# Kernel tuning notes

Hardware: AMD Instinct MI355X
Metric: run time of the kernel (lower is better)

Reference implementation:

```python
import jax, jax.numpy as jnp
import numpy as np

DIM = 256
N_EMBED = 8192


def setup_inputs() -> dict:
    key = jax.random.key(0)
    k1, k2 = jax.random.split(key)
    inp = jax.random.normal(k1, (8, 4096, DIM), dtype=jnp.float32)
    embed = jax.random.normal(k2, (DIM, N_EMBED), dtype=jnp.float32)  # codebook [dim, n_embed]
    return {"input": inp, "embed": embed}


def reference(input, embed):
    # Flatten all leading dims into N code queries: [N, dim]
    flatten = input.reshape(-1, DIM)
    dist = (
        jnp.sum(flatten * flatten, axis=1, keepdims=True)
        - 2.0 * (flatten @ embed)
        + jnp.sum(embed * embed, axis=0, keepdims=True)
    )
    # (-dist).max(1) indices == argmin of dist
    embed_ind = jnp.argmin(dist, axis=1).reshape(input.shape[:-1])  # [B, T]
    # Embedding gather from codebook transpose: [B, T, dim]
    quantize = jnp.take(embed.T, embed_ind, axis=0)
    # Commitment loss (quantize detached)
    diff = jnp.mean(jnp.square(jax.lax.stop_gradient(quantize) - input))
    # Straight-through estimator
    quantize = input + jax.lax.stop_gradient(quantize - input)
    return quantize, diff, embed_ind
```

## Files before the change

### kernel.cpp

```cpp
#include <hip/hip_runtime.h>

#define DIM 256
#define NEMB 8192
#define NQ 32768
#define OUT_Q_ELEMS 8388608
#define NSEG 2
#define SEG_CODES 4096
#define CAP_H 32
#define MARGIN 1.0f

typedef __attribute__((ext_vector_type(8))) short short8;
typedef __attribute__((ext_vector_type(4))) float f32x4;
typedef unsigned int u32_as1 __attribute__((address_space(1)));
typedef unsigned int u32_as3 __attribute__((address_space(3)));

__device__ __forceinline__ unsigned short f2bf(float f) {
    unsigned u = __float_as_uint(f);
    u += 0x7FFFu + ((u >> 16) & 1u);
    return (unsigned short)(u >> 16);
}
__device__ __forceinline__ void gll16(const void* g, void* l) {
    __builtin_amdgcn_global_load_lds((const u32_as1*)g, (u32_as3*)l, 16, 0, 0);
}

__global__ void prep_kernel(const float* __restrict__ input,
                            const float* __restrict__ embed,
                            int* __restrict__ cnt2, double* __restrict__ ed,
                            float* __restrict__ ef, float* __restrict__ ebt,
                            unsigned short* __restrict__ Xc,
                            unsigned short* __restrict__ Ec,
                            double* __restrict__ pacc) {
    __shared__ float t[64][65];
    const int b = blockIdx.x;
    if (b < 512) {
        cnt2[b * 256 + threadIdx.x] = 0;
    } else if (b < 544) {
        if (b == 512 && threadIdx.x < 64) pacc[threadIdx.x] = 0.0;
        int j = (b - 512) * 256 + threadIdx.x;
        double s = 0.0;
        for (int d = 0; d < DIM; ++d) {
            double v = (double)embed[(size_t)d * NEMB + j];
            s += v * v;
        }
        ed[j] = s;
        ef[j] = (float)s;
    } else if (b < 1056) {
        const int bb = b - 544;
        const int bx = bb & 127, by = bb >> 7;
        const int tx = threadIdx.x & 63, ty = threadIdx.x >> 6;
#pragma unroll
        for (int i = 0; i < 16; ++i) {
            int d = by * 64 + ty * 16 + i;
            t[ty * 16 + i][tx] = embed[(size_t)d * NEMB + bx * 64 + tx];
        }
        __syncthreads();
#pragma unroll
        for (int i = 0; i < 16; ++i) {
            int c = bx * 64 + ty * 16 + i;
            ebt[(size_t)c * DIM + by * 64 + tx] = t[tx][ty * 16 + i];
        }
    } else if (b < 5152) {
        int tid = (b - 1056) * 256 + threadIdx.x;
        int q = tid >> 5, kcc = tid & 31;
        const float* p = input + (size_t)q * DIM + kcc * 8;
        float4 a = *(const float4*)p;
        float4 bv = *(const float4*)(p + 4);
        int mb = q >> 7, mrow = q & 127, kc = kcc >> 3, c = kcc & 7;
        short8 v;
        v[0] = (short)f2bf(a.x);  v[1] = (short)f2bf(a.y);
        v[2] = (short)f2bf(a.z);  v[3] = (short)f2bf(a.w);
        v[4] = (short)f2bf(bv.x); v[5] = (short)f2bf(bv.y);
        v[6] = (short)f2bf(bv.z); v[7] = (short)f2bf(bv.w);
        *(short8*)(Xc + (size_t)((((mb * 4 + kc) * 8) + c) * 128 + mrow) * 8) = v;
    } else {
        int tid = (b - 5152) * 256 + threadIdx.x;
        int n = tid & (NEMB - 1), kcc = tid >> 13;
        int nb = n >> 7, nrow = n & 127, kc = kcc >> 3, c = kcc & 7;
        short8 v;
#pragma unroll
        for (int j = 0; j < 8; ++j)
            v[j] = (short)f2bf(embed[(size_t)(kc * 64 + c * 8 + j) * NEMB + n]);
        *(short8*)(Ec + (size_t)((((nb * 4 + kc) * 8) + c) * 128 + nrow) * 8) = v;
    }
}

__global__ __launch_bounds__(512, 4) void mfma_argmin_kernel(
    const unsigned short* __restrict__ Xc, const unsigned short* __restrict__ Ec,
    const float* __restrict__ ef, int* __restrict__ cnt2,
    unsigned short* __restrict__ cand) {
    __shared__ unsigned short As[32768];
    __shared__ unsigned short Bs[2][4096];

    const int tid = threadIdx.x;
    const int w = tid >> 6, l = tid & 63;
    const int wm = w >> 1, wn = w & 1;
    const int l15 = l & 15, q4 = l >> 4;
    const int mb = blockIdx.x & 255;
    const int seg = blockIdx.x >> 8;

    const unsigned short* xt = Xc + (size_t)mb * 32768;
    const unsigned short* Eseg = Ec + ((size_t)seg << 20);

#pragma unroll
    for (int s = 0; s < 8; ++s) {
        const int t = w * 8 + s;
        gll16(xt + t * 512 + l * 8, &As[t * 512 + l * 8]);
    }
    gll16(Eseg + w * 512 + l * 8, &Bs[0][w * 512 + l * 8]);
    asm volatile("s_waitcnt vmcnt(0)" ::: "memory");
    asm volatile("s_barrier" ::: "memory");

    float rmax[2][4];
    int   rcnt[2][4];
#pragma unroll
    for (int i = 0; i < 2; ++i)
#pragma unroll
        for (int r = 0; r < 4; ++r) { rmax[i][r] = -1e30f; rcnt[i][r] = 0; }

    for (int t16 = 0; t16 < 32; ++t16) {
        const int nb = seg * 32 + t16;
        const int col0 = nb * 128 + wn * 64 + l15;
        float enh[4];
#pragma unroll
        for (int j = 0; j < 4; ++j) enh[j] = 0.5f * ef[col0 + 16 * j];

        f32x4 acc[2][4];
#pragma unroll
        for (int i = 0; i < 2; ++i)
#pragma unroll
            for (int j = 0; j < 4; ++j) acc[i][j] = (f32x4){0.f, 0.f, 0.f, 0.f};

#pragma unroll
        for (int c8 = 0; c8 < 8; ++c8) {
            const int nc = t16 * 8 + c8 + 1;
            if (nc < 256)
                gll16(Eseg + ((size_t)nc << 12) + w * 512 + l * 8,
                      &Bs[nc & 1][w * 512 + l * 8]);

            const int kc = c8 >> 1, h = c8 & 1;
            short8 af[2], bf[4];
#pragma unroll
            for (int i = 0; i < 2; ++i)
                af[i] = *(const short8*)&As[kc * 8192 +
                    ((h * 4 + q4) * 128 + wm * 32 + i * 16 + l15) * 8];
#pragma unroll
            for (int j = 0; j < 4; ++j)
                bf[j] = *(const short8*)&Bs[h][
                    (q4 * 128 + wn * 64 + j * 16 + l15) * 8];

            __builtin_amdgcn_s_setprio(1);
#pragma unroll
            for (int i = 0; i < 2; ++i)
#pragma unroll
                for (int j = 0; j < 4; ++j)
                    acc[i][j] = __builtin_amdgcn_mfma_f32_16x16x32_bf16(
                        af[i], bf[j], acc[i][j], 0, 0, 0);
            __builtin_amdgcn_s_setprio(0);

            if (c8 == 7) {
#pragma unroll
                for (int i = 0; i < 2; ++i)
#pragma unroll
                    for (int r = 0; r < 4; ++r) {
                        const float s0 = acc[i][0][r] - enh[0];
                        const float s1 = acc[i][1][r] - enh[1];
                        const float s2 = acc[i][2][r] - enh[2];
                        const float s3 = acc[i][3][r] - enh[3];
                        float M = fmaxf(fmaxf(fmaxf(s0, s1), fmaxf(s2, s3)),
                                        rmax[i][r]);
#pragma unroll
                        for (int step = 1; step < 16; step <<= 1)
                            M = fmaxf(M, __shfl_xor(M, step, 64));
                        rmax[i][r] = M;
                        const float tau = M - 0.5f * MARGIN;
                        const float sm = fmaxf(fmaxf(s0, s1), fmaxf(s2, s3));
                        const unsigned long long bb = __ballot(sm > tau);
                        const unsigned g = (unsigned)(bb >> (q4 * 16)) & 0xFFFFu;
                        if (g) {
                            int base = rcnt[i][r];
                            const int row128 = wm * 32 + i * 16 + q4 * 4 + r;
                            const size_t cb =
                                ((size_t)((mb * 128 + row128) * NSEG + seg) * 2 +
                                 wn) * CAP_H;
                            const float sj[4] = {s0, s1, s2, s3};
#pragma unroll
                            for (int j = 0; j < 4; ++j) {
                                const bool cdd = sj[j] > tau;
                                const unsigned long long bj = __ballot(cdd);
                                const unsigned gj =
                                    (unsigned)(bj >> (q4 * 16)) & 0xFFFFu;
                                if (cdd) {
                                    int slot =
                                        base + __popc(gj & ((1u << l15) - 1u));
                                    if (slot < CAP_H)
                                        cand[cb + slot] =
                                            (unsigned short)(col0 + 16 * j);
                                }
                                base += __popc(gj);
                            }
                            rcnt[i][r] = base;
                        }
                    }
            }
            asm volatile("s_waitcnt vmcnt(0)" ::: "memory");
            asm volatile("s_barrier" ::: "memory");
        }
    }
    if (l15 == 0) {
#pragma unroll
        for (int i = 0; i < 2; ++i)
#pragma unroll
            for (int r = 0; r < 4; ++r) {
                const int row128 = wm * 32 + i * 16 + q4 * 4 + r;
                cnt2[((mb * 128 + row128) * NSEG + seg) * 2 + wn] = rcnt[i][r];
            }
    }
}

__global__ __launch_bounds__(256) void rescore_kernel(
    const float* __restrict__ input, const float* __restrict__ ebt,
    const double* __restrict__ ed, const int* __restrict__ cnt2,
    const unsigned short* __restrict__ cand, float* __restrict__ out_q,
    float* __restrict__ out_idx, double* __restrict__ pacc) {
    __shared__ float Xs[4][DIM];
    __shared__ double dred[4];
    const int w = threadIdx.x >> 6, l = threadIdx.x & 63;
    const int g = l >> 2, sub = l & 3;

    double ddw = 0.0;
    for (int it = 0; it < 4; ++it) {
        const int q = (blockIdx.x * 4 + w) * 4 + it;

        float4 xf = *(const float4*)(input + (size_t)q * DIM + 4 * l);
        *(float4*)&Xs[w][4 * l] = xf;

        int m[4];
        bool ss[NSEG];
#pragma unroll
        for (int s2 = 0; s2 < NSEG; ++s2) ss[s2] = false;
#pragma unroll
        for (int li = 0; li < 4; ++li) {
            int ns = cnt2[(q * NSEG + (li >> 1)) * 2 + (li & 1)];
            if (ns > CAP_H) ss[li >> 1] = true;
            m[li] = ns;
        }
#pragma unroll
        for (int li = 0; li < 4; ++li)
            if (ss[li >> 1]) m[li] = 0;
        const int tot = m[0] + m[1] + m[2] + m[3];

        int bc;
        if (!ss[0] && !ss[1] && tot == 1) {
            int li = 0;
#pragma unroll
            for (int li2 = 0; li2 < 3; ++li2)
                if (m[li] == 0) ++li;
            bc = cand[((size_t)(q * NSEG + (li >> 1)) * 2 + (li & 1)) * CAP_H];
        } else {
            double bd = 1e300;
            bc = 0x7FFFFFFF;
            const float* xsub = &Xs[w][sub * 64];

            for (int base = 0; base < tot; base += 16) {
                const int idx = base + g;
                int c = -1;
                if (idx < tot) {
                    int rem = idx, li = 0;
#pragma unroll
                    for (int li2 = 0; li2 < 3; ++li2)
                        if (rem >= m[li]) { rem -= m[li]; ++li; }
                    c = cand[((size_t)(q * NSEG + (li >> 1)) * 2 + (li & 1)) *
                                 CAP_H + rem];
                }
                if (c >= 0) {
                    const float* ep = ebt + (size_t)c * DIM + sub * 64;
                    float accf = 0.f;
#pragma unroll
                    for (int t = 0; t < 16; ++t) {
                        float4 e4 = *(const float4*)(ep + 4 * t);
                        float4 x4 = *(const float4*)(xsub + 4 * t);
                        accf = fmaf(x4.x, e4.x, accf);
                        accf = fmaf(x4.y, e4.y, accf);
                        accf = fmaf(x4.z, e4.z, accf);
                        accf = fmaf(x4.w, e4.w, accf);
                    }
                    double p = (double)accf;
                    p += __shfl_xor(p, 1, 64);
                    p += __shfl_xor(p, 2, 64);
                    const double dist = ed[c] - 2.0 * p;
                    if (dist < bd || (dist == bd && c < bc)) {
                        bd = dist; bc = c;
                    }
                }
            }
#pragma unroll
            for (int s2 = 0; s2 < NSEG; ++s2) {
                if (ss[s2]) {
                    for (int b2 = 0; b2 < SEG_CODES; b2 += 16) {
                        const int c = s2 * SEG_CODES + b2 + g;
                        const float* ep = ebt + (size_t)c * DIM + sub * 64;
                        float accf = 0.f;
#pragma unroll
                        for (int t = 0; t < 16; ++t) {
                            float4 e4 = *(const float4*)(ep + 4 * t);
                            float4 x4 = *(const float4*)(xsub + 4 * t);
                            accf = fmaf(x4.x, e4.x, accf);
                            accf = fmaf(x4.y, e4.y, accf);
                            accf = fmaf(x4.z, e4.z, accf);
                            accf = fmaf(x4.w, e4.w, accf);
                        }
                        double p = (double)accf;
                        p += __shfl_xor(p, 1, 64);
                        p += __shfl_xor(p, 2, 64);
                        const double dist = ed[c] - 2.0 * p;
                        if (dist < bd || (dist == bd && c < bc)) {
                            bd = dist; bc = c;
                        }
                    }
                }
            }
#pragma unroll
            for (int off = 4; off < 64; off <<= 1) {
                double od = __shfl_xor(bd, off, 64);
                int oc = __shfl_xor(bc, off, 64);
                if (od < bd || (od == bd && oc < bc)) { bd = od; bc = oc; }
            }
        }

        float4 e4 = *(const float4*)(ebt + (size_t)bc * DIM + 4 * l);
        *(float4*)(out_q + (size_t)q * DIM + 4 * l) = e4;
        float d0 = e4.x - xf.x, d1 = e4.y - xf.y;
        float d2 = e4.z - xf.z, d3 = e4.w - xf.w;
        double dd = (double)d0 * d0 + (double)d1 * d1 +
                    (double)d2 * d2 + (double)d3 * d3;
#pragma unroll
        for (int off = 1; off < 64; off <<= 1) dd += __shfl_xor(dd, off, 64);
        if (l == 0) out_idx[q] = (float)bc;
        ddw += dd;
    }

    if (l == 0) dred[w] = ddw;
    __syncthreads();
    if (threadIdx.x == 0)
        atomicAdd(pacc + (blockIdx.x & 63),
                  dred[0] + dred[1] + dred[2] + dred[3]);
}

__global__ void diff_kernel(const double* __restrict__ pacc,
                            float* __restrict__ out_diff) {
    const int t = threadIdx.x;
    double s = pacc[t];
#pragma unroll
    for (int off = 32; off >= 1; off >>= 1) s += __shfl_down(s, off, 64);
    if (t == 0)
        out_diff[0] = (float)(s / (double)OUT_Q_ELEMS);
}

extern "C" void kernel_launch(void* const* d_in, const int* in_sizes, int n_in,
                              void* d_out, int out_size, void* d_ws,
                              size_t ws_size, hipStream_t stream) {
    const float* input = (const float*)d_in[0];
    const float* embed = (const float*)d_in[1];

    float* out_q    = (float*)d_out;
    float* out_diff = out_q + OUT_Q_ELEMS;
    float* out_idx  = out_diff + 1;

    char* p = (char*)d_ws;
    unsigned short* Ec  = (unsigned short*)(p);
    unsigned short* Xc  = (unsigned short*)(p + 4194304);
    float*          ebt = (float*)(p + 20971520);
    double*         ed  = (double*)(p + 29360128);
    float*          ef  = (float*)(p + 29425664);
    int*            cnt2 = (int*)(p + 29458432);
    double*         pacc = (double*)(p + 29982720);
    unsigned short* cand = (unsigned short*)(p + 30244864);

    hipLaunchKernelGGL(prep_kernel, dim3(6176), dim3(256), 0, stream,
                       input, embed, cnt2, ed, ef, ebt, Xc, Ec, pacc);
    hipLaunchKernelGGL(mfma_argmin_kernel, dim3((NQ / 128) * NSEG), dim3(512),
                       0, stream, Xc, Ec, ef, cnt2, cand);
    hipLaunchKernelGGL(rescore_kernel, dim3(NQ / 16), dim3(256), 0, stream,
                       input, ebt, ed, cnt2, cand, out_q, out_idx, pacc);
    hipLaunchKernelGGL(diff_kernel, dim3(1), dim3(64), 0, stream,
                       pacc, out_diff);
}
```

Measured before the change: 400.9 us.

## Prune rescore candidates using stored bf16 scores against the global row max

The argmin kernel now writes each candidate's approximate bf16 score and the per-row running max to workspace. The rescore kernel compacts candidates into shared memory, keeping only those within half the margin of the global row max across segments and halves. When a single candidate survives it skips the exact fp32/fp64 rescoring. This trades extra global writes of scores and maxima for fewer exact dot products. The tighter threshold could drop the true argmin if the bf16 error bound is exceeded.

```diff
diff --git a/kernel.cpp b/kernel.cpp
--- a/kernel.cpp
+++ b/kernel.cpp
@@ -87,7 +87,8 @@
 __global__ __launch_bounds__(512, 4) void mfma_argmin_kernel(
     const unsigned short* __restrict__ Xc, const unsigned short* __restrict__ Ec,
     const float* __restrict__ ef, int* __restrict__ cnt2,
-    unsigned short* __restrict__ cand) {
+    unsigned short* __restrict__ cand, float* __restrict__ cands,
+    float* __restrict__ rmaxg) {
     __shared__ unsigned short As[32768];
     __shared__ unsigned short Bs[2][4096];
 
@@ -192,9 +193,11 @@
                                 if (cdd) {
                                     int slot =
                                         base + __popc(gj & ((1u << l15) - 1u));
-                                    if (slot < CAP_H)
+                                    if (slot < CAP_H) {
                                         cand[cb + slot] =
                                             (unsigned short)(col0 + 16 * j);
+                                        cands[cb + slot] = sj[j];
+                                    }
                                 }
                                 base += __popc(gj);
                             }
@@ -212,7 +215,9 @@
 #pragma unroll
             for (int r = 0; r < 4; ++r) {
                 const int row128 = wm * 32 + i * 16 + q4 * 4 + r;
-                cnt2[((mb * 128 + row128) * NSEG + seg) * 2 + wn] = rcnt[i][r];
+                const int idx = ((mb * 128 + row128) * NSEG + seg) * 2 + wn;
+                cnt2[idx] = rcnt[i][r];
+                rmaxg[idx] = rmax[i][r];
             }
     }
 }
@@ -220,9 +225,11 @@
 __global__ __launch_bounds__(256) void rescore_kernel(
     const float* __restrict__ input, const float* __restrict__ ebt,
     const double* __restrict__ ed, const int* __restrict__ cnt2,
-    const unsigned short* __restrict__ cand, float* __restrict__ out_q,
+    const unsigned short* __restrict__ cand, const float* __restrict__ cands,
+    const float* __restrict__ rmaxg, float* __restrict__ out_q,
     float* __restrict__ out_idx, double* __restrict__ pacc) {
     __shared__ float Xs[4][DIM];
+    __shared__ unsigned short Ks[4][128];
     __shared__ double dred[4];
     const int w = threadIdx.x >> 6, l = threadIdx.x & 63;
     const int g = l >> 2, sub = l & 3;
@@ -232,35 +239,96 @@
         const int q = (blockIdx.x * 4 + w) * 4 + it;
 
         float4 xf = *(const float4*)(input + (size_t)q * DIM + 4 * l);
-        *(float4*)&Xs[w][4 * l] = xf;
-
-        int m[4];
-        bool ss[NSEG];
-#pragma unroll
-        for (int s2 = 0; s2 < NSEG; ++s2) ss[s2] = false;
-#pragma unroll
-        for (int li = 0; li < 4; ++li) {
-            int ns = cnt2[(q * NSEG + (li >> 1)) * 2 + (li & 1)];
-            if (ns > CAP_H) ss[li >> 1] = true;
-            m[li] = ns;
-        }
+
+        const int4 mc = *(const int4*)(cnt2 + q * 4);
+        const float4 Mv = *(const float4*)(rmaxg + q * 4);
+        int m[4] = {mc.x, mc.y, mc.z, mc.w};
+        const float Mg =
+            fmaxf(fmaxf(Mv.x, Mv.y), fmaxf(Mv.z, Mv.w));
+        bool ss[NSEG] = {false, false};
 #pragma unroll
         for (int li = 0; li < 4; ++li)
-            if (ss[li >> 1]) m[li] = 0;
-        const int tot = m[0] + m[1] + m[2] + m[3];
-
-        int bc;
-        if (!ss[0] && !ss[1] && tot == 1) {
-            int li = 0;
-#pragma unroll
-            for (int li2 = 0; li2 < 3; ++li2)
-                if (m[li] == 0) ++li;
-            bc = cand[((size_t)(q * NSEG + (li >> 1)) * 2 + (li & 1)) * CAP_H];
+            if (m[li] > CAP_H) ss[li >> 1] = true;
+
+        int bc = -1;
+        const bool ovf = ss[0] || ss[1];
+
+        if (!ovf) {
+            const int tot = m[0] + m[1] + m[2] + m[3];
+            const float tau = Mg - 0.5f * MARGIN;
+            int nk = 0;
+            for (int base = 0; base < tot; base += 64) {
+                const int idx = base + l;
+                int c = -1;
+                float s = -1e30f;
+                if (idx < tot) {
+                    int rem = idx, li = 0;
+#pragma unroll
+                    for (int li2 = 0; li2 < 3; ++li2)
+                        if (rem >= m[li]) { rem -= m[li]; ++li; }
+                    const size_t off =
+                        ((size_t)(q * NSEG + (li >> 1)) * 2 + (li & 1)) *
+                            CAP_H + rem;
+                    c = cand[off];
+                    s = cands[off];
+                }
+                const bool keep = (c >= 0) && (s >= tau);
+                const unsigned long long kb = __ballot(keep);
+                if (keep) {
+                    const int slot =
+                        nk + __popcll(kb & ((1ull << l) - 1ull));
+                    Ks[w][slot] = (unsigned short)c;
+                }
+                nk += __popcll(kb);
+            }
+            if (nk == 1) {
+                bc = Ks[w][0];
+            } else {
+                *(float4*)&Xs[w][4 * l] = xf;
+                const float* xsub = &Xs[w][sub * 64];
+                double bd = 1e300;
+                int bbc = 0x7FFFFFFF;
+                for (int base = 0; base < nk; base += 16) {
+                    const int kidx = base + g;
+                    const int c = (kidx < nk) ? (int)Ks[w][kidx] : -1;
+                    if (c >= 0) {
+                        const float* ep = ebt + (size_t)c * DIM + sub * 64;
+                        float accf = 0.f;
+#pragma unroll
+                        for (int t = 0; t < 16; ++t) {
+                            float4 e4 = *(const float4*)(ep + 4 * t);
+                            float4 x4 = *(const float4*)(xsub + 4 * t);
+                            accf = fmaf(x4.x, e4.x, accf);
+                            accf = fmaf(x4.y, e4.y, accf);
+                            accf = fmaf(x4.z, e4.z, accf);
+                            accf = fmaf(x4.w, e4.w, accf);
+                        }
+                        double p = (double)accf;
+                        p += __shfl_xor(p, 1, 64);
+                        p += __shfl_xor(p, 2, 64);
+                        const double dist = ed[c] - 2.0 * p;
+                        if (dist < bd || (dist == bd && c < bbc)) {
+                            bd = dist; bbc = c;
+                        }
+                    }
+                }
+#pragma unroll
+                for (int off = 4; off < 64; off <<= 1) {
+                    double od = __shfl_xor(bd, off, 64);
+                    int oc = __shfl_xor(bbc, off, 64);
+                    if (od < bd || (od == bd && oc < bbc)) { bd = od; bbc = oc; }
+                }
+                bc = bbc;
+            }
         } else {
+#pragma unroll
+            for (int li = 0; li < 4; ++li)
+                if (ss[li >> 1]) m[li] = 0;
+            const int tot = m[0] + m[1] + m[2] + m[3];
+            *(float4*)&Xs[w][4 * l] = xf;
+            const float* xsub = &Xs[w][sub * 64];
             double bd = 1e300;
-            bc = 0x7FFFFFFF;
-            const float* xsub = &Xs[w][sub * 64];
-
+            int bbc = 0x7FFFFFFF;
             for (int base = 0; base < tot; base += 16) {
                 const int idx = base + g;
                 int c = -1;
@@ -288,8 +356,8 @@
                     p += __shfl_xor(p, 1, 64);
                     p += __shfl_xor(p, 2, 64);
                     const double dist = ed[c] - 2.0 * p;
-                    if (dist < bd || (dist == bd && c < bc)) {
-                        bd = dist; bc = c;
+                    if (dist < bd || (dist == bd && c < bbc)) {
+                        bd = dist; bbc = c;
                     }
                 }
             }
@@ -313,8 +381,8 @@
                         p += __shfl_xor(p, 1, 64);
                         p += __shfl_xor(p, 2, 64);
                         const double dist = ed[c] - 2.0 * p;
-                        if (dist < bd || (dist == bd && c < bc)) {
-                            bd = dist; bc = c;
+                        if (dist < bd || (dist == bd && c < bbc)) {
+                            bd = dist; bbc = c;
                         }
                     }
                 }
@@ -322,9 +390,10 @@
 #pragma unroll
             for (int off = 4; off < 64; off <<= 1) {
                 double od = __shfl_xor(bd, off, 64);
-                int oc = __shfl_xor(bc, off, 64);
-                if (od < bd || (od == bd && oc < bc)) { bd = od; bc = oc; }
-            }
+                int oc = __shfl_xor(bbc, off, 64);
+                if (od < bd || (od == bd && oc < bbc)) { bd = od; bbc = oc; }
+            }
+            bc = bbc;
         }
 
         float4 e4 = *(const float4*)(ebt + (size_t)bc * DIM + 4 * l);
@@ -367,21 +436,24 @@
     float* out_idx  = out_diff + 1;
 
     char* p = (char*)d_ws;
-    unsigned short* Ec  = (unsigned short*)(p);
-    unsigned short* Xc  = (unsigned short*)(p + 4194304);
-    float*          ebt = (float*)(p + 20971520);
-    double*         ed  = (double*)(p + 29360128);
-    float*          ef  = (float*)(p + 29425664);
+    unsigned short* Ec   = (unsigned short*)(p);
+    unsigned short* Xc   = (unsigned short*)(p + 4194304);
+    float*          ebt  = (float*)(p + 20971520);
+    double*         ed   = (double*)(p + 29360128);
+    float*          ef   = (float*)(p + 29425664);
     int*            cnt2 = (int*)(p + 29458432);
     double*         pacc = (double*)(p + 29982720);
-    unsigned short* cand = (unsigned short*)(p + 30244864);
+    float*          rmaxg = (float*)(p + 29986816);
+    unsigned short* cand = (unsigned short*)(p + 30511104);
+    float*          cands = (float*)(p + 38899712);
 
     hipLaunchKernelGGL(prep_kernel, dim3(6176), dim3(256), 0, stream,
                        input, embed, cnt2, ed, ef, ebt, Xc, Ec, pacc);
     hipLaunchKernelGGL(mfma_argmin_kernel, dim3((NQ / 128) * NSEG), dim3(512),
-                       0, stream, Xc, Ec, ef, cnt2, cand);
+                       0, stream, Xc, Ec, ef, cnt2, cand, cands, rmaxg);
     hipLaunchKernelGGL(rescore_kernel, dim3(NQ / 16), dim3(256), 0, stream,
-                       input, ebt, ed, cnt2, cand, out_q, out_idx, pacc);
+                       input, ebt, ed, cnt2, cand, cands, rmaxg,
+                       out_q, out_idx, pacc);
     hipLaunchKernelGGL(diff_kernel, dim3(1), dim3(64), 0, stream,
                        pacc, out_diff);
 }
```

After: 336.1 us. 16.2% less time.
